# Performance work log

Hardware: AMD Instinct MI355X
Metric: run time of the kernel (lower is better)

## Reference

```python
import jax, jax.numpy as jnp
import numpy as np

SR = 10  # self.sr in the torch module

def _linear_params(key, fan_in, fan_out):
    kw, kb = jax.random.split(key)
    bound = 1.0 / np.sqrt(fan_in)
    W = jax.random.uniform(kw, (fan_out, fan_in), jnp.float32, -bound, bound)
    b = jax.random.uniform(kb, (fan_out,), jnp.float32, -bound, bound)
    return W, b

def setup_inputs() -> dict:
    key = jax.random.key(0)
    ks = jax.random.split(key, 6)
    P, H = 2048, 1024
    R = C = P * SR
    X = jax.random.normal(ks[0], (R, C), jnp.float32)
    p = jax.random.randint(ks[1], (P,), 0, 64, jnp.int32)
    W1, b1 = _linear_params(ks[2], 1, H)
    W2, b2 = _linear_params(ks[3], H, H)
    W3, b3 = _linear_params(ks[4], H, H)
    W4, b4 = _linear_params(ks[5], H, 1)
    return {"X": X, "p": p, "W1": W1, "b1": b1, "W2": W2, "b2": b2,
            "W3": W3, "b3": b3, "W4": W4, "b4": b4}

def _forward(X, p, W1, b1, W2, b2, W3, b3, W4, b4):
    P = p.shape[0]
    C = X.shape[1]
    # shift_rows: only rows i*SR for i in [0, P-2] are populated; all other
    # rows of the shifted matrix are NaN and contribute 0 sum / 0 count below.
    rows = X[jnp.arange(P - 1) * SR]                      # (P-1, C)
    shifts = p[: P - 1]
    # torch.roll(x, s): out[j] = x[(j - s) mod C]
    cols = (jnp.arange(C)[None, :] - shifts[:, None]) % C  # (P-1, C)
    shifted = jnp.take_along_axis(rows, cols, axis=1)      # (P-1, C)
    # nan_mean over rows (NaN rows of the full matrix drop out identically)
    mask = jnp.isnan(shifted)
    col_sum = jnp.where(mask, 0.0, shifted).sum(axis=0)
    col_cnt = (~mask).sum(axis=0).astype(jnp.float32)
    m = jnp.where(col_cnt > 0, col_sum / col_cnt, jnp.float32(jnp.nan))  # (C,)
    # fill_nan_with_last_value: serial forward-fill (index 0 kept as-is)
    def step(last, xi):
        v = jnp.where(jnp.isnan(xi), last, xi)
        return v, v
    _, rest = jax.lax.scan(step, m[0], m[1:])
    filled = jnp.concatenate([m[:1], rest])                # (C,)
    x = filled[::SR][:P][:, None]                          # (P, 1)
    h = jax.nn.relu(x @ W1.T + b1)
    h = jax.nn.relu(h @ W2.T + b2)
    h = jax.nn.relu(h @ W3.T + b3)
    y = h @ W4.T + b4                                      # (P, 1)
    return y[:, 0]

def reference(X, p, W1, b1, W2, b2, W3, b3, W4, b4):
    return _forward(X, p, W1, b1, W2, b2, W3, b3, W4, b4)
```

## Files before the change

kernel.cpp:

```cpp
#include <hip/hip_runtime.h>
#include <hip/hip_bf16.h>

#define CC 20480
#define PP 2048
#define NROWS 2047
#define SRR 10
#define HH 1024
#define NCH 64

typedef __attribute__((ext_vector_type(8))) short short8;
typedef __attribute__((ext_vector_type(4))) float f32x4;

__device__ __forceinline__ void split_bf16(float v, unsigned short& hi, unsigned short& lo) {
    __hip_bfloat16 h = __float2bfloat16(v);
    float r = v - __bfloat162float(h);
    __hip_bfloat16 l2 = __float2bfloat16(r);
    hi = *(unsigned short*)&h;
    lo = *(unsigned short*)&l2;
}

__global__ __launch_bounds__(256) void pre_k(const float* __restrict__ X,
                                             const int* __restrict__ p,
                                             float* __restrict__ psum,
                                             const float* __restrict__ W2,
                                             unsigned short* __restrict__ w2h,
                                             unsigned short* __restrict__ w2l,
                                             const float* __restrict__ W3,
                                             unsigned short* __restrict__ w3h,
                                             unsigned short* __restrict__ w3l) {
    int b = blockIdx.x, t = threadIdx.x;
    if (b < 512) {
        int k = (b & 7) * 256 + t;
        int chunk = b >> 3;
        int r0 = chunk * 32;
        int r1 = r0 + 32; if (r1 > NROWS) r1 = NROWS;
        float s = 0.f;
        int base = SRR * k;
        for (int i = r0; i < r1; ++i) {
            int col = base - p[i]; if (col < 0) col += CC;
            s += X[(size_t)i * (size_t)(SRR * CC) + col];
        }
        psum[chunk * PP + k] = s;
        return;
    }
    int bb = b - 512;
    const float* src; unsigned short *dh, *dl;
    if (bb < 256) { src = W2; dh = w2h; dl = w2l; }
    else { src = W3; dh = w3h; dl = w3l; bb -= 256; }
    int idx = bb * 4096 + t * 16;
    #pragma unroll
    for (int q = 0; q < 4; ++q) {
        float4 v = *(const float4*)&src[idx + q * 4];
        float vv[4] = {v.x, v.y, v.z, v.w};
        ushort hi4[4], lo4[4];
        #pragma unroll
        for (int i = 0; i < 4; ++i) split_bf16(vv[i], hi4[i], lo4[i]);
        *(ushort4*)&dh[idx + q * 4] = *(ushort4*)hi4;
        *(ushort4*)&dl[idx + q * 4] = *(ushort4*)lo4;
    }
}

__device__ __forceinline__ void gload16(const unsigned short* g, unsigned short* lds) {
    __builtin_amdgcn_global_load_lds(
        (const __attribute__((address_space(1))) void*)g,
        (__attribute__((address_space(3))) void*)lds,
        16, 0, 0);
}

#define BM 128
#define BN 64
#define BK 64

__global__ __launch_bounds__(512, 2) void gemm1_k(
    const float* __restrict__ psum,
    const float* __restrict__ W1, const float* __restrict__ b1,
    const unsigned short* __restrict__ Bh, const unsigned short* __restrict__ Bl,
    const float* __restrict__ b2,
    unsigned short* __restrict__ Ch, unsigned short* __restrict__ Cl)
{
    __shared__ unsigned short Bb[3][8192];
    __shared__ float w1f[1024], b1f[1024], xv[128];

    int lin = blockIdx.x;
    int v = (lin & 7) * 32 + (lin >> 3);
    int bx = v >> 4, by = v & 15;
    int bm = bx * BM, bn = by * BN;
    int t = threadIdx.x, w = t >> 6, l = t & 63;
    int lr = l & 15, lk = l >> 4;
    int wr = w >> 1, wc = w & 1;

    size_t offB = (size_t)(bn + (w >> 1) * 16 + lr) * HH + (w & 1) * 32 + lk * 8;
#define BSTAGE(buf, k0)                                         \
    do {                                                        \
        gload16(Bh + offB + (k0), Bb[buf] + w * 512);           \
        gload16(Bl + offB + (k0), Bb[buf] + 4096 + w * 512);    \
    } while (0)

    BSTAGE(0, 0);
    {
        int row = t >> 2, q = t & 3;
        float s = 0.f;
        #pragma unroll
        for (int j = 0; j < 16; ++j) s += psum[(q * 16 + j) * PP + bm + row];
        s += __shfl_xor(s, 1, 64);
        s += __shfl_xor(s, 2, 64);
        if (q == 0) xv[row] = s * (1.0f / (float)NROWS);
        if (t < 256) *(float4*)&w1f[t * 4] = *(const float4*)&W1[t * 4];
        else *(float4*)&b1f[(t - 256) * 4] = *(const float4*)&b1[(t - 256) * 4];
    }
    __syncthreads();

    float x0 = xv[wr * 32 + lr], x1 = xv[wr * 32 + 16 + lr];

    f32x4 acc[2][2];
    #pragma unroll
    for (int i = 0; i < 2; ++i)
        #pragma unroll
        for (int j = 0; j < 2; ++j) acc[i][j] = (f32x4)(0.f);

    int nt = HH / BK;
    for (int tt = 0; tt < nt; ++tt) {
        int cur = tt % 3;
        if (tt + 1 < nt) {
            BSTAGE((tt + 1) % 3, (tt + 1) * BK);
            asm volatile("s_waitcnt vmcnt(2)" ::: "memory");
        } else {
            asm volatile("s_waitcnt vmcnt(0)" ::: "memory");
        }
        __builtin_amdgcn_s_barrier();
        __builtin_amdgcn_sched_barrier(0);
        __builtin_amdgcn_s_setprio(1);
        #pragma unroll
        for (int s2 = 0; s2 < 2; ++s2) {
            int k0 = tt * BK + s2 * 32;
            float4 wva = *(const float4*)&w1f[k0 + lk * 8];
            float4 wvb = *(const float4*)&w1f[k0 + lk * 8 + 4];
            float4 bva = *(const float4*)&b1f[k0 + lk * 8];
            float4 bvb = *(const float4*)&b1f[k0 + lk * 8 + 4];
            float wv[8] = {wva.x, wva.y, wva.z, wva.w, wvb.x, wvb.y, wvb.z, wvb.w};
            float bv2[8] = {bva.x, bva.y, bva.z, bva.w, bvb.x, bvb.y, bvb.z, bvb.w};
            ushort ahh[2][8], all2[2][8];
            #pragma unroll
            for (int mi = 0; mi < 2; ++mi) {
                float xm = mi ? x1 : x0;
                #pragma unroll
                for (int j = 0; j < 8; ++j) {
                    float h = fmaf(xm, wv[j], bv2[j]);
                    h = h > 0.f ? h : 0.f;
                    split_bf16(h, ahh[mi][j], all2[mi][j]);
                }
            }
            short8 bh2[2], bl2[2];
            #pragma unroll
            for (int ni = 0; ni < 2; ++ni) {
                bh2[ni] = *(const short8*)&Bb[cur][((wc * 2 + ni) * 2 + s2) * 512 + l * 8];
                bl2[ni] = *(const short8*)&Bb[cur][4096 + ((wc * 2 + ni) * 2 + s2) * 512 + l * 8];
            }
            #pragma unroll
            for (int mi = 0; mi < 2; ++mi) {
                short8 ah2 = *(short8*)ahh[mi];
                short8 al2 = *(short8*)all2[mi];
                #pragma unroll
                for (int ni = 0; ni < 2; ++ni) {
                    acc[mi][ni] = __builtin_amdgcn_mfma_f32_16x16x32_bf16(ah2, bh2[ni], acc[mi][ni], 0, 0, 0);
                    acc[mi][ni] = __builtin_amdgcn_mfma_f32_16x16x32_bf16(ah2, bl2[ni], acc[mi][ni], 0, 0, 0);
                    acc[mi][ni] = __builtin_amdgcn_mfma_f32_16x16x32_bf16(al2, bh2[ni], acc[mi][ni], 0, 0, 0);
                }
            }
        }
        __builtin_amdgcn_s_setprio(0);
        __builtin_amdgcn_sched_barrier(0);
    }
#undef BSTAGE

    float bv[2];
    #pragma unroll
    for (int ni = 0; ni < 2; ++ni) bv[ni] = b2[bn + wc * 32 + ni * 16 + lr];
    #pragma unroll
    for (int mi = 0; mi < 2; ++mi)
        #pragma unroll
        for (int ni = 0; ni < 2; ++ni)
            #pragma unroll
            for (int r = 0; r < 4; ++r) {
                int row = bm + wr * 32 + mi * 16 + lk * 4 + r;
                int col = bn + wc * 32 + ni * 16 + lr;
                float vv = acc[mi][ni][r] + bv[ni];
                vv = vv > 0.f ? vv : 0.f;
                unsigned short hi, lo;
                split_bf16(vv, hi, lo);
                Ch[(size_t)row * HH + col] = hi;
                Cl[(size_t)row * HH + col] = lo;
            }
}

__global__ __launch_bounds__(512, 2) void gemm2_k(
    const unsigned short* __restrict__ Ah, const unsigned short* __restrict__ Al,
    const unsigned short* __restrict__ Bh, const unsigned short* __restrict__ Bl,
    const float* __restrict__ b3,
    const float* __restrict__ W4, float* __restrict__ partial)
{
    __shared__ unsigned short lds[3][24576];
    int lin = blockIdx.x;
    int v = (lin & 7) * 32 + (lin >> 3);
    int bx = v >> 4, by = v & 15;
    int bm = bx * BM, bn = by * BN;
    int t = threadIdx.x, w = t >> 6, l = t & 63;
    int lr = l & 15, lk = l >> 4;
    int wr = w >> 1, wc = w & 1;

    size_t offA = (size_t)(bm + w * 16 + lr) * HH + lk * 8;
    size_t offB = (size_t)(bn + (w & 3) * 16 + lr) * HH + lk * 8;

#define STAGE(buf, k0)                                                          \
    do {                                                                        \
        unsigned short* L = lds[buf];                                           \
        gload16(Ah + offA + (k0),      L + (w * 2 + 0) * 512);                  \
        gload16(Ah + offA + (k0) + 32, L + (w * 2 + 1) * 512);                  \
        gload16(Al + offA + (k0),      L + 8192 + (w * 2 + 0) * 512);           \
        gload16(Al + offA + (k0) + 32, L + 8192 + (w * 2 + 1) * 512);           \
        if (w < 4) {                                                            \
            gload16(Bh + offB + (k0),      L + 16384 + ((w & 3) * 2 + 0) * 512);\
            gload16(Bh + offB + (k0) + 32, L + 16384 + ((w & 3) * 2 + 1) * 512);\
        } else {                                                                \
            gload16(Bl + offB + (k0),      L + 20480 + ((w & 3) * 2 + 0) * 512);\
            gload16(Bl + offB + (k0) + 32, L + 20480 + ((w & 3) * 2 + 1) * 512);\
        }                                                                       \
    } while (0)

    f32x4 acc[2][2];
    #pragma unroll
    for (int i = 0; i < 2; ++i)
        #pragma unroll
        for (int j = 0; j < 2; ++j) acc[i][j] = (f32x4)(0.f);

    STAGE(0, 0);

    int nt = HH / BK;
    for (int tt = 0; tt < nt; ++tt) {
        int cur = tt % 3;
        if (tt + 1 < nt) {
            STAGE((tt + 1) % 3, (tt + 1) * BK);
            asm volatile("s_waitcnt vmcnt(6)" ::: "memory");
        } else {
            asm volatile("s_waitcnt vmcnt(0)" ::: "memory");
        }
        __builtin_amdgcn_s_barrier();
        __builtin_amdgcn_sched_barrier(0);
        __builtin_amdgcn_s_setprio(1);
        unsigned short* L = lds[cur];
        #pragma unroll
        for (int s2 = 0; s2 < 2; ++s2) {
            short8 ah2[2], al2[2], bh2[2], bl2[2];
            #pragma unroll
            for (int mi = 0; mi < 2; ++mi) {
                ah2[mi] = *(const short8*)&L[((wr * 2 + mi) * 2 + s2) * 512 + l * 8];
                al2[mi] = *(const short8*)&L[8192 + ((wr * 2 + mi) * 2 + s2) * 512 + l * 8];
            }
            #pragma unroll
            for (int ni = 0; ni < 2; ++ni) {
                bh2[ni] = *(const short8*)&L[16384 + ((wc * 2 + ni) * 2 + s2) * 512 + l * 8];
                bl2[ni] = *(const short8*)&L[20480 + ((wc * 2 + ni) * 2 + s2) * 512 + l * 8];
            }
            #pragma unroll
            for (int mi = 0; mi < 2; ++mi)
                #pragma unroll
                for (int ni = 0; ni < 2; ++ni) {
                    acc[mi][ni] = __builtin_amdgcn_mfma_f32_16x16x32_bf16(ah2[mi], bh2[ni], acc[mi][ni], 0, 0, 0);
                    acc[mi][ni] = __builtin_amdgcn_mfma_f32_16x16x32_bf16(ah2[mi], bl2[ni], acc[mi][ni], 0, 0, 0);
                    acc[mi][ni] = __builtin_amdgcn_mfma_f32_16x16x32_bf16(al2[mi], bh2[ni], acc[mi][ni], 0, 0, 0);
                }
        }
        __builtin_amdgcn_s_setprio(0);
        __builtin_amdgcn_sched_barrier(0);
    }
#undef STAGE

    float bv[2], w4v[2];
    #pragma unroll
    for (int ni = 0; ni < 2; ++ni) {
        bv[ni]  = b3[bn + wc * 32 + ni * 16 + lr];
        w4v[ni] = W4[bn + wc * 32 + ni * 16 + lr];
    }
    #pragma unroll
    for (int mi = 0; mi < 2; ++mi) {
        float ps[4];
        #pragma unroll
        for (int r = 0; r < 4; ++r) {
            float acc_d = 0.f;
            #pragma unroll
            for (int ni = 0; ni < 2; ++ni) {
                float vv = acc[mi][ni][r] + bv[ni];
                vv = vv > 0.f ? vv : 0.f;
                acc_d += vv * w4v[ni];
            }
            ps[r] = acc_d;
        }
        #pragma unroll
        for (int r = 0; r < 4; ++r) {
            #pragma unroll
            for (int m2 = 1; m2 < 16; m2 <<= 1) ps[r] += __shfl_xor(ps[r], m2, 64);
        }
        if (lr == 0) {
            #pragma unroll
            for (int r = 0; r < 4; ++r) {
                int row = bm + wr * 32 + mi * 16 + lk * 4 + r;
                partial[(size_t)row * 32 + by * 2 + wc] = ps[r];
            }
        }
    }
}

__global__ __launch_bounds__(256) void ysum_k(const float* __restrict__ partial,
                                              const float* __restrict__ b4,
                                              float* __restrict__ y) {
    int r = blockIdx.x * 256 + threadIdx.x;
    float s = 0.f;
    #pragma unroll
    for (int q = 0; q < 8; ++q) {
        float4 v = *(const float4*)&partial[(size_t)r * 32 + q * 4];
        s += v.x + v.y + v.z + v.w;
    }
    y[r] = s + b4[0];
}

extern "C" void kernel_launch(void* const* d_in, const int* in_sizes, int n_in,
                              void* d_out, int out_size, void* d_ws, size_t ws_size,
                              hipStream_t stream) {
    const float* X  = (const float*)d_in[0];
    const int*   p  = (const int*)d_in[1];
    const float* W1 = (const float*)d_in[2];
    const float* b1 = (const float*)d_in[3];
    const float* W2 = (const float*)d_in[4];
    const float* b2 = (const float*)d_in[5];
    const float* W3 = (const float*)d_in[6];
    const float* b3 = (const float*)d_in[7];
    const float* W4 = (const float*)d_in[8];
    const float* b4 = (const float*)d_in[9];
    float* out = (float*)d_out;

    char* ws = (char*)d_ws;
    size_t off = 0;
    float* psum = (float*)(ws + off); off += (size_t)NCH * PP * 4;
    unsigned short* h2h = (unsigned short*)(ws + off); off += (size_t)PP * HH * 2;
    unsigned short* h2l = (unsigned short*)(ws + off); off += (size_t)PP * HH * 2;
    unsigned short* w2h = (unsigned short*)(ws + off); off += (size_t)HH * HH * 2;
    unsigned short* w2l = (unsigned short*)(ws + off); off += (size_t)HH * HH * 2;
    unsigned short* w3h = (unsigned short*)(ws + off); off += (size_t)HH * HH * 2;
    unsigned short* w3l = (unsigned short*)(ws + off); off += (size_t)HH * HH * 2;
    float* partial = (float*)(ws + off); off += (size_t)PP * 32 * 4;

    pre_k<<<1024, 256, 0, stream>>>(X, p, psum, W2, w2h, w2l, W3, w3h, w3l);
    gemm1_k<<<256, 512, 0, stream>>>(psum, W1, b1, w2h, w2l, b2, h2h, h2l);
    gemm2_k<<<256, 512, 0, stream>>>(h2h, h2l, w3h, w3l, b3, W4, partial);
    ysum_k<<<PP / 256, 256, 0, stream>>>(partial, b4, out);
}
```

Measured before the change: 80.19 us.

## Move W3 bf16 split into gemm1 launch and deepen GEMM prefetch to two stages

After: 83.76 us. 4.5% more time.

```diff
diff --git a/kernel.cpp b/kernel.cpp
--- a/kernel.cpp
+++ b/kernel.cpp
@@ -24,10 +24,7 @@
                                              float* __restrict__ psum,
                                              const float* __restrict__ W2,
                                              unsigned short* __restrict__ w2h,
-                                             unsigned short* __restrict__ w2l,
-                                             const float* __restrict__ W3,
-                                             unsigned short* __restrict__ w3h,
-                                             unsigned short* __restrict__ w3l) {
+                                             unsigned short* __restrict__ w2l) {
     int b = blockIdx.x, t = threadIdx.x;
     if (b < 512) {
         int k = (b & 7) * 256 + t;
@@ -44,19 +41,16 @@
         return;
     }
     int bb = b - 512;
-    const float* src; unsigned short *dh, *dl;
-    if (bb < 256) { src = W2; dh = w2h; dl = w2l; }
-    else { src = W3; dh = w3h; dl = w3l; bb -= 256; }
     int idx = bb * 4096 + t * 16;
     #pragma unroll
     for (int q = 0; q < 4; ++q) {
-        float4 v = *(const float4*)&src[idx + q * 4];
+        float4 v = *(const float4*)&W2[idx + q * 4];
         float vv[4] = {v.x, v.y, v.z, v.w};
         ushort hi4[4], lo4[4];
         #pragma unroll
         for (int i = 0; i < 4; ++i) split_bf16(vv[i], hi4[i], lo4[i]);
-        *(ushort4*)&dh[idx + q * 4] = *(ushort4*)hi4;
-        *(ushort4*)&dl[idx + q * 4] = *(ushort4*)lo4;
+        *(ushort4*)&w2h[idx + q * 4] = *(ushort4*)hi4;
+        *(ushort4*)&w2l[idx + q * 4] = *(ushort4*)lo4;
     }
 }
 
@@ -76,16 +70,33 @@
     const float* __restrict__ W1, const float* __restrict__ b1,
     const unsigned short* __restrict__ Bh, const unsigned short* __restrict__ Bl,
     const float* __restrict__ b2,
-    unsigned short* __restrict__ Ch, unsigned short* __restrict__ Cl)
+    unsigned short* __restrict__ Ch, unsigned short* __restrict__ Cl,
+    const float* __restrict__ W3,
+    unsigned short* __restrict__ w3h, unsigned short* __restrict__ w3l)
 {
     __shared__ unsigned short Bb[3][8192];
     __shared__ float w1f[1024], b1f[1024], xv[128];
 
-    int lin = blockIdx.x;
+    int lin = blockIdx.x, t = threadIdx.x;
+    if (lin >= 256) {
+        int bb = lin - 256;
+        int idx = bb * 4096 + t * 8;
+        #pragma unroll
+        for (int q = 0; q < 2; ++q) {
+            float4 v = *(const float4*)&W3[idx + q * 4];
+            float vv[4] = {v.x, v.y, v.z, v.w};
+            ushort hi4[4], lo4[4];
+            #pragma unroll
+            for (int i = 0; i < 4; ++i) split_bf16(vv[i], hi4[i], lo4[i]);
+            *(ushort4*)&w3h[idx + q * 4] = *(ushort4*)hi4;
+            *(ushort4*)&w3l[idx + q * 4] = *(ushort4*)lo4;
+        }
+        return;
+    }
     int v = (lin & 7) * 32 + (lin >> 3);
     int bx = v >> 4, by = v & 15;
     int bm = bx * BM, bn = by * BN;
-    int t = threadIdx.x, w = t >> 6, l = t & 63;
+    int w = t >> 6, l = t & 63;
     int lr = l & 15, lk = l >> 4;
     int wr = w >> 1, wc = w & 1;
 
@@ -97,6 +108,7 @@
     } while (0)
 
     BSTAGE(0, 0);
+    BSTAGE(1, BK);
     {
         int row = t >> 2, q = t & 3;
         float s = 0.f;
@@ -121,14 +133,11 @@
     int nt = HH / BK;
     for (int tt = 0; tt < nt; ++tt) {
         int cur = tt % 3;
-        if (tt + 1 < nt) {
-            BSTAGE((tt + 1) % 3, (tt + 1) * BK);
-            asm volatile("s_waitcnt vmcnt(2)" ::: "memory");
-        } else {
-            asm volatile("s_waitcnt vmcnt(0)" ::: "memory");
-        }
+        if (tt + 1 < nt) asm volatile("s_waitcnt vmcnt(2)" ::: "memory");
+        else             asm volatile("s_waitcnt vmcnt(0)" ::: "memory");
         __builtin_amdgcn_s_barrier();
         __builtin_amdgcn_sched_barrier(0);
+        if (tt + 2 < nt) BSTAGE((tt + 2) % 3, (tt + 2) * BK);
         __builtin_amdgcn_s_setprio(1);
         #pragma unroll
         for (int s2 = 0; s2 < 2; ++s2) {
@@ -234,18 +243,16 @@
         for (int j = 0; j < 2; ++j) acc[i][j] = (f32x4)(0.f);
 
     STAGE(0, 0);
+    STAGE(1, BK);
 
     int nt = HH / BK;
     for (int tt = 0; tt < nt; ++tt) {
         int cur = tt % 3;
-        if (tt + 1 < nt) {
-            STAGE((tt + 1) % 3, (tt + 1) * BK);
-            asm volatile("s_waitcnt vmcnt(6)" ::: "memory");
-        } else {
-            asm volatile("s_waitcnt vmcnt(0)" ::: "memory");
-        }
+        if (tt + 1 < nt) asm volatile("s_waitcnt vmcnt(6)" ::: "memory");
+        else             asm volatile("s_waitcnt vmcnt(0)" ::: "memory");
         __builtin_amdgcn_s_barrier();
         __builtin_amdgcn_sched_barrier(0);
+        if (tt + 2 < nt) STAGE((tt + 2) % 3, (tt + 2) * BK);
         __builtin_amdgcn_s_setprio(1);
         unsigned short* L = lds[cur];
         #pragma unroll
@@ -349,8 +356,8 @@
     unsigned short* w3l = (unsigned short*)(ws + off); off += (size_t)HH * HH * 2;
     float* partial = (float*)(ws + off); off += (size_t)PP * 32 * 4;
 
-    pre_k<<<1024, 256, 0, stream>>>(X, p, psum, W2, w2h, w2l, W3, w3h, w3l);
-    gemm1_k<<<256, 512, 0, stream>>>(psum, W1, b1, w2h, w2l, b2, h2h, h2l);
+    pre_k<<<768, 256, 0, stream>>>(X, p, psum, W2, w2h, w2l);
+    gemm1_k<<<512, 512, 0, stream>>>(psum, W1, b1, w2h, w2l, b2, h2h, h2l, W3, w3h, w3l);
     gemm2_k<<<256, 512, 0, stream>>>(h2h, h2l, w3h, w3l, b3, W4, partial);
     ysum_k<<<PP / 256, 256, 0, stream>>>(partial, b4, out);
 }
```

## Fuse all four stages into one cooperative kernel with grid-wide syncs

Applied to the files above, without the earlier changes.

Result: slower. 185.1 us (+130.9%).

```diff
diff --git a/kernel.cpp b/kernel.cpp
--- a/kernel.cpp
+++ b/kernel.cpp
@@ -1,5 +1,8 @@
 #include <hip/hip_runtime.h>
+#include <hip/hip_cooperative_groups.h>
 #include <hip/hip_bf16.h>
+
+namespace cg = cooperative_groups;
 
 #define CC 20480
 #define PP 2048
@@ -19,19 +22,37 @@
     lo = *(unsigned short*)&l2;
 }
 
-__global__ __launch_bounds__(256) void pre_k(const float* __restrict__ X,
-                                             const int* __restrict__ p,
-                                             float* __restrict__ psum,
-                                             const float* __restrict__ W2,
-                                             unsigned short* __restrict__ w2h,
-                                             unsigned short* __restrict__ w2l,
-                                             const float* __restrict__ W3,
-                                             unsigned short* __restrict__ w3h,
-                                             unsigned short* __restrict__ w3l) {
+__device__ __forceinline__ void gload16(const unsigned short* g, unsigned short* lds) {
+    __builtin_amdgcn_global_load_lds(
+        (const __attribute__((address_space(1))) void*)g,
+        (__attribute__((address_space(3))) void*)lds,
+        16, 0, 0);
+}
+
+#define BM 128
+#define BN 64
+#define BK 64
+
+__global__ __launch_bounds__(512, 1) void fused_k(
+    const float* __restrict__ X, const int* __restrict__ p,
+    float* __restrict__ psum,
+    const float* __restrict__ W1, const float* __restrict__ b1,
+    const float* __restrict__ W2, const float* __restrict__ b2,
+    const float* __restrict__ W3, const float* __restrict__ b3,
+    const float* __restrict__ W4, const float* __restrict__ b4,
+    unsigned short* __restrict__ w2h, unsigned short* __restrict__ w2l,
+    unsigned short* __restrict__ w3h, unsigned short* __restrict__ w3l,
+    unsigned short* __restrict__ h2h, unsigned short* __restrict__ h2l,
+    float* __restrict__ partial, float* __restrict__ out)
+{
+    __shared__ unsigned short LDSU[3][24576];
+    cg::grid_group grid = cg::this_grid();
     int b = blockIdx.x, t = threadIdx.x;
-    if (b < 512) {
-        int k = (b & 7) * 256 + t;
-        int chunk = b >> 3;
+    int tid = b * 512 + t;
+
+    {
+        int k = tid & 2047;
+        int chunk = tid >> 11;
         int r0 = chunk * 32;
         int r1 = r0 + 32; if (r1 > NROWS) r1 = NROWS;
         float s = 0.f;
@@ -41,286 +62,265 @@
             s += X[(size_t)i * (size_t)(SRR * CC) + col];
         }
         psum[chunk * PP + k] = s;
-        return;
+        int idx = tid * 8;
+        #pragma unroll
+        for (int q = 0; q < 2; ++q) {
+            float4 v2 = *(const float4*)&W2[idx + q * 4];
+            float4 v3 = *(const float4*)&W3[idx + q * 4];
+            float a2[4] = {v2.x, v2.y, v2.z, v2.w};
+            float a3[4] = {v3.x, v3.y, v3.z, v3.w};
+            ushort h24[4], l24[4], h34[4], l34[4];
+            #pragma unroll
+            for (int i = 0; i < 4; ++i) {
+                split_bf16(a2[i], h24[i], l24[i]);
+                split_bf16(a3[i], h34[i], l34[i]);
+            }
+            *(ushort4*)&w2h[idx + q * 4] = *(ushort4*)h24;
+            *(ushort4*)&w2l[idx + q * 4] = *(ushort4*)l24;
+            *(ushort4*)&w3h[idx + q * 4] = *(ushort4*)h34;
+            *(ushort4*)&w3l[idx + q * 4] = *(ushort4*)l34;
+        }
     }
-    int bb = b - 512;
-    const float* src; unsigned short *dh, *dl;
-    if (bb < 256) { src = W2; dh = w2h; dl = w2l; }
-    else { src = W3; dh = w3h; dl = w3l; bb -= 256; }
-    int idx = bb * 4096 + t * 16;
-    #pragma unroll
-    for (int q = 0; q < 4; ++q) {
-        float4 v = *(const float4*)&src[idx + q * 4];
-        float vv[4] = {v.x, v.y, v.z, v.w};
-        ushort hi4[4], lo4[4];
-        #pragma unroll
-        for (int i = 0; i < 4; ++i) split_bf16(vv[i], hi4[i], lo4[i]);
-        *(ushort4*)&dh[idx + q * 4] = *(ushort4*)hi4;
-        *(ushort4*)&dl[idx + q * 4] = *(ushort4*)lo4;
+    grid.sync();
+
+    {
+        unsigned short* BbF = &LDSU[0][0];
+        float* w1f = (float*)(BbF + 3 * 8192);
+        float* b1f = w1f + 1024;
+        float* xv  = b1f + 1024;
+
+        int v = (b & 7) * 32 + (b >> 3);
+        int bx = v >> 4, by = v & 15;
+        int bm = bx * BM, bn = by * BN;
+        int w = t >> 6, l = t & 63;
+        int lr = l & 15, lk = l >> 4;
+        int wr = w >> 1, wc = w & 1;
+
+        size_t offB = (size_t)(bn + (w >> 1) * 16 + lr) * HH + (w & 1) * 32 + lk * 8;
+#define BSTAGE(buf, k0)                                                \
+        do {                                                           \
+            gload16(w2h + offB + (k0), BbF + (buf) * 8192 + w * 512);  \
+            gload16(w2l + offB + (k0), BbF + (buf) * 8192 + 4096 + w * 512); \
+        } while (0)
+
+        BSTAGE(0, 0);
+        {
+            int row = t >> 2, q = t & 3;
+            float s = 0.f;
+            #pragma unroll
+            for (int j = 0; j < 16; ++j) s += psum[(q * 16 + j) * PP + bm + row];
+            s += __shfl_xor(s, 1, 64);
+            s += __shfl_xor(s, 2, 64);
+            if (q == 0) xv[row] = s * (1.0f / (float)NROWS);
+            if (t < 256) *(float4*)&w1f[t * 4] = *(const float4*)&W1[t * 4];
+            else *(float4*)&b1f[(t - 256) * 4] = *(const float4*)&b1[(t - 256) * 4];
+        }
+        __syncthreads();
+
+        float x0 = xv[wr * 32 + lr], x1 = xv[wr * 32 + 16 + lr];
+
+        f32x4 acc[2][2];
+        #pragma unroll
+        for (int i = 0; i < 2; ++i)
+            #pragma unroll
+            for (int j = 0; j < 2; ++j) acc[i][j] = (f32x4)(0.f);
+
+        int nt = HH / BK;
+        for (int tt = 0; tt < nt; ++tt) {
+            int cur = tt % 3;
+            if (tt + 1 < nt) {
+                BSTAGE((tt + 1) % 3, (tt + 1) * BK);
+                asm volatile("s_waitcnt vmcnt(2)" ::: "memory");
+            } else {
+                asm volatile("s_waitcnt vmcnt(0)" ::: "memory");
+            }
+            __builtin_amdgcn_s_barrier();
+            __builtin_amdgcn_sched_barrier(0);
+            __builtin_amdgcn_s_setprio(1);
+            #pragma unroll
+            for (int s2 = 0; s2 < 2; ++s2) {
+                int k0 = tt * BK + s2 * 32;
+                float4 wva = *(const float4*)&w1f[k0 + lk * 8];
+                float4 wvb = *(const float4*)&w1f[k0 + lk * 8 + 4];
+                float4 bva = *(const float4*)&b1f[k0 + lk * 8];
+                float4 bvb = *(const float4*)&b1f[k0 + lk * 8 + 4];
+                float wv[8] = {wva.x, wva.y, wva.z, wva.w, wvb.x, wvb.y, wvb.z, wvb.w};
+                float bv2[8] = {bva.x, bva.y, bva.z, bva.w, bvb.x, bvb.y, bvb.z, bvb.w};
+                ushort ahh[2][8], all2[2][8];
+                #pragma unroll
+                for (int mi = 0; mi < 2; ++mi) {
+                    float xm = mi ? x1 : x0;
+                    #pragma unroll
+                    for (int j = 0; j < 8; ++j) {
+                        float h = fmaf(xm, wv[j], bv2[j]);
+                        h = h > 0.f ? h : 0.f;
+                        split_bf16(h, ahh[mi][j], all2[mi][j]);
+                    }
+                }
+                short8 bh2[2], bl2[2];
+                #pragma unroll
+                for (int ni = 0; ni < 2; ++ni) {
+                    bh2[ni] = *(const short8*)&BbF[cur * 8192 + ((wc * 2 + ni) * 2 + s2) * 512 + l * 8];
+                    bl2[ni] = *(const short8*)&BbF[cur * 8192 + 4096 + ((wc * 2 + ni) * 2 + s2) * 512 + l * 8];
+                }
+                #pragma unroll
+                for (int mi = 0; mi < 2; ++mi) {
+                    short8 ah2 = *(short8*)ahh[mi];
+                    short8 al2 = *(short8*)all2[mi];
+                    #pragma unroll
+                    for (int ni = 0; ni < 2; ++ni) {
+                        acc[mi][ni] = __builtin_amdgcn_mfma_f32_16x16x32_bf16(ah2, bh2[ni], acc[mi][ni], 0, 0, 0);
+                        acc[mi][ni] = __builtin_amdgcn_mfma_f32_16x16x32_bf16(ah2, bl2[ni], acc[mi][ni], 0, 0, 0);
+                        acc[mi][ni] = __builtin_amdgcn_mfma_f32_16x16x32_bf16(al2, bh2[ni], acc[mi][ni], 0, 0, 0);
+                    }
+                }
+            }
+            __builtin_amdgcn_s_setprio(0);
+            __builtin_amdgcn_sched_barrier(0);
+        }
+#undef BSTAGE
+
+        float bv[2];
+        #pragma unroll
+        for (int ni = 0; ni < 2; ++ni) bv[ni] = b2[bn + wc * 32 + ni * 16 + lr];
+        #pragma unroll
+        for (int mi = 0; mi < 2; ++mi)
+            #pragma unroll
+            for (int ni = 0; ni < 2; ++ni)
+                #pragma unroll
+                for (int r = 0; r < 4; ++r) {
+                    int row = bm + wr * 32 + mi * 16 + lk * 4 + r;
+                    int col = bn + wc * 32 + ni * 16 + lr;
+                    float vv = acc[mi][ni][r] + bv[ni];
+                    vv = vv > 0.f ? vv : 0.f;
+                    unsigned short hi, lo;
+                    split_bf16(vv, hi, lo);
+                    h2h[(size_t)row * HH + col] = hi;
+                    h2l[(size_t)row * HH + col] = lo;
+                }
     }
-}
-
-__device__ __forceinline__ void gload16(const unsigned short* g, unsigned short* lds) {
-    __builtin_amdgcn_global_load_lds(
-        (const __attribute__((address_space(1))) void*)g,
-        (__attribute__((address_space(3))) void*)lds,
-        16, 0, 0);
-}
-
-#define BM 128
-#define BN 64
-#define BK 64
-
-__global__ __launch_bounds__(512, 2) void gemm1_k(
-    const float* __restrict__ psum,
-    const float* __restrict__ W1, const float* __restrict__ b1,
-    const unsigned short* __restrict__ Bh, const unsigned short* __restrict__ Bl,
-    const float* __restrict__ b2,
-    unsigned short* __restrict__ Ch, unsigned short* __restrict__ Cl)
-{
-    __shared__ unsigned short Bb[3][8192];
-    __shared__ float w1f[1024], b1f[1024], xv[128];
-
-    int lin = blockIdx.x;
-    int v = (lin & 7) * 32 + (lin >> 3);
-    int bx = v >> 4, by = v & 15;
-    int bm = bx * BM, bn = by * BN;
-    int t = threadIdx.x, w = t >> 6, l = t & 63;
-    int lr = l & 15, lk = l >> 4;
-    int wr = w >> 1, wc = w & 1;
-
-    size_t offB = (size_t)(bn + (w >> 1) * 16 + lr) * HH + (w & 1) * 32 + lk * 8;
-#define BSTAGE(buf, k0)                                         \
-    do {                                                        \
-        gload16(Bh + offB + (k0), Bb[buf] + w * 512);           \
-        gload16(Bl + offB + (k0), Bb[buf] + 4096 + w * 512);    \
-    } while (0)
-
-    BSTAGE(0, 0);
+    grid.sync();
+
     {
-        int row = t >> 2, q = t & 3;
+        int v = (b & 7) * 32 + (b >> 3);
+        int bx = v >> 4, by = v & 15;
+        int bm = bx * BM, bn = by * BN;
+        int w = t >> 6, l = t & 63;
+        int lr = l & 15, lk = l >> 4;
+        int wr = w >> 1, wc = w & 1;
+
+        size_t offA = (size_t)(bm + w * 16 + lr) * HH + lk * 8;
+        size_t offB = (size_t)(bn + (w & 3) * 16 + lr) * HH + lk * 8;
+
+#define STAGE(buf, k0)                                                              \
+        do {                                                                        \
+            unsigned short* L = LDSU[buf];                                          \
+            gload16(h2h + offA + (k0),      L + (w * 2 + 0) * 512);                 \
+            gload16(h2h + offA + (k0) + 32, L + (w * 2 + 1) * 512);                 \
+            gload16(h2l + offA + (k0),      L + 8192 + (w * 2 + 0) * 512);          \
+            gload16(h2l + offA + (k0) + 32, L + 8192 + (w * 2 + 1) * 512);          \
+            if (w < 4) {                                                            \
+                gload16(w3h + offB + (k0),      L + 16384 + ((w & 3) * 2 + 0) * 512);\
+                gload16(w3h + offB + (k0) + 32, L + 16384 + ((w & 3) * 2 + 1) * 512);\
+            } else {                                                                \
+                gload16(w3l + offB + (k0),      L + 20480 + ((w & 3) * 2 + 0) * 512);\
+                gload16(w3l + offB + (k0) + 32, L + 20480 + ((w & 3) * 2 + 1) * 512);\
+            }                                                                       \
+        } while (0)
+
+        f32x4 acc[2][2];
+        #pragma unroll
+        for (int i = 0; i < 2; ++i)
+            #pragma unroll
+            for (int j = 0; j < 2; ++j) acc[i][j] = (f32x4)(0.f);
+
+        STAGE(0, 0);
+
+        int nt = HH / BK;
+        for (int tt = 0; tt < nt; ++tt) {
+            int cur = tt % 3;
+            if (tt + 1 < nt) {
+                STAGE((tt + 1) % 3, (tt + 1) * BK);
+                asm volatile("s_waitcnt vmcnt(6)" ::: "memory");
+            } else {
+                asm volatile("s_waitcnt vmcnt(0)" ::: "memory");
+            }
+            __builtin_amdgcn_s_barrier();
+            __builtin_amdgcn_sched_barrier(0);
+            __builtin_amdgcn_s_setprio(1);
+            unsigned short* L = LDSU[cur];
+            #pragma unroll
+            for (int s2 = 0; s2 < 2; ++s2) {
+                short8 ah2[2], al2[2], bh2[2], bl2[2];
+                #pragma unroll
+                for (int mi = 0; mi < 2; ++mi) {
+                    ah2[mi] = *(const short8*)&L[((wr * 2 + mi) * 2 + s2) * 512 + l * 8];
+                    al2[mi] = *(const short8*)&L[8192 + ((wr * 2 + mi) * 2 + s2) * 512 + l * 8];
+                }
+                #pragma unroll
+                for (int ni = 0; ni < 2; ++ni) {
+                    bh2[ni] = *(const short8*)&L[16384 + ((wc * 2 + ni) * 2 + s2) * 512 + l * 8];
+                    bl2[ni] = *(const short8*)&L[20480 + ((wc * 2 + ni) * 2 + s2) * 512 + l * 8];
+                }
+                #pragma unroll
+                for (int mi = 0; mi < 2; ++mi)
+                    #pragma unroll
+                    for (int ni = 0; ni < 2; ++ni) {
+                        acc[mi][ni] = __builtin_amdgcn_mfma_f32_16x16x32_bf16(ah2[mi], bh2[ni], acc[mi][ni], 0, 0, 0);
+                        acc[mi][ni] = __builtin_amdgcn_mfma_f32_16x16x32_bf16(ah2[mi], bl2[ni], acc[mi][ni], 0, 0, 0);
+                        acc[mi][ni] = __builtin_amdgcn_mfma_f32_16x16x32_bf16(al2[mi], bh2[ni], acc[mi][ni], 0, 0, 0);
+                    }
+            }
+            __builtin_amdgcn_s_setprio(0);
+            __builtin_amdgcn_sched_barrier(0);
+        }
+#undef STAGE
+
+        float bv[2], w4v[2];
+        #pragma unroll
+        for (int ni = 0; ni < 2; ++ni) {
+            bv[ni]  = b3[bn + wc * 32 + ni * 16 + lr];
+            w4v[ni] = W4[bn + wc * 32 + ni * 16 + lr];
+        }
+        #pragma unroll
+        for (int mi = 0; mi < 2; ++mi) {
+            float ps[4];
+            #pragma unroll
+            for (int r = 0; r < 4; ++r) {
+                float acc_d = 0.f;
+                #pragma unroll
+                for (int ni = 0; ni < 2; ++ni) {
+                    float vv = acc[mi][ni][r] + bv[ni];
+                    vv = vv > 0.f ? vv : 0.f;
+                    acc_d += vv * w4v[ni];
+                }
+                ps[r] = acc_d;
+            }
+            #pragma unroll
+            for (int r = 0; r < 4; ++r) {
+                #pragma unroll
+                for (int m2 = 1; m2 < 16; m2 <<= 1) ps[r] += __shfl_xor(ps[r], m2, 64);
+            }
+            if (lr == 0) {
+                #pragma unroll
+                for (int r = 0; r < 4; ++r) {
+                    int row = bm + wr * 32 + mi * 16 + lk * 4 + r;
+                    partial[(size_t)row * 32 + by * 2 + wc] = ps[r];
+                }
+            }
+        }
+    }
+    grid.sync();
+
+    if (tid < PP) {
         float s = 0.f;
         #pragma unroll
-        for (int j = 0; j < 16; ++j) s += psum[(q * 16 + j) * PP + bm + row];
-        s += __shfl_xor(s, 1, 64);
-        s += __shfl_xor(s, 2, 64);
-        if (q == 0) xv[row] = s * (1.0f / (float)NROWS);
-        if (t < 256) *(float4*)&w1f[t * 4] = *(const float4*)&W1[t * 4];
-        else *(float4*)&b1f[(t - 256) * 4] = *(const float4*)&b1[(t - 256) * 4];
+        for (int q = 0; q < 8; ++q) {
+            float4 v = *(const float4*)&partial[(size_t)tid * 32 + q * 4];
+            s += v.x + v.y + v.z + v.w;
+        }
+        out[tid] = s + b4[0];
     }
-    __syncthreads();
-
-    float x0 = xv[wr * 32 + lr], x1 = xv[wr * 32 + 16 + lr];
-
-    f32x4 acc[2][2];
-    #pragma unroll
-    for (int i = 0; i < 2; ++i)
-        #pragma unroll
-        for (int j = 0; j < 2; ++j) acc[i][j] = (f32x4)(0.f);
-
-    int nt = HH / BK;
-    for (int tt = 0; tt < nt; ++tt) {
-        int cur = tt % 3;
-        if (tt + 1 < nt) {
-            BSTAGE((tt + 1) % 3, (tt + 1) * BK);
-            asm volatile("s_waitcnt vmcnt(2)" ::: "memory");
-        } else {
-            asm volatile("s_waitcnt vmcnt(0)" ::: "memory");
-        }
-        __builtin_amdgcn_s_barrier();
-        __builtin_amdgcn_sched_barrier(0);
-        __builtin_amdgcn_s_setprio(1);
-        #pragma unroll
-        for (int s2 = 0; s2 < 2; ++s2) {
-            int k0 = tt * BK + s2 * 32;
-            float4 wva = *(const float4*)&w1f[k0 + lk * 8];
-            float4 wvb = *(const float4*)&w1f[k0 + lk * 8 + 4];
-            float4 bva = *(const float4*)&b1f[k0 + lk * 8];
-            float4 bvb = *(const float4*)&b1f[k0 + lk * 8 + 4];
-            float wv[8] = {wva.x, wva.y, wva.z, wva.w, wvb.x, wvb.y, wvb.z, wvb.w};
-            float bv2[8] = {bva.x, bva.y, bva.z, bva.w, bvb.x, bvb.y, bvb.z, bvb.w};
-            ushort ahh[2][8], all2[2][8];
-            #pragma unroll
-            for (int mi = 0; mi < 2; ++mi) {
-                float xm = mi ? x1 : x0;
-                #pragma unroll
-                for (int j = 0; j < 8; ++j) {
-                    float h = fmaf(xm, wv[j], bv2[j]);
-                    h = h > 0.f ? h : 0.f;
-                    split_bf16(h, ahh[mi][j], all2[mi][j]);
-                }
-            }
-            short8 bh2[2], bl2[2];
-            #pragma unroll
-            for (int ni = 0; ni < 2; ++ni) {
-                bh2[ni] = *(const short8*)&Bb[cur][((wc * 2 + ni) * 2 + s2) * 512 + l * 8];
-                bl2[ni] = *(const short8*)&Bb[cur][4096 + ((wc * 2 + ni) * 2 + s2) * 512 + l * 8];
-            }
-            #pragma unroll
-            for (int mi = 0; mi < 2; ++mi) {
-                short8 ah2 = *(short8*)ahh[mi];
-                short8 al2 = *(short8*)all2[mi];
-                #pragma unroll
-                for (int ni = 0; ni < 2; ++ni) {
-                    acc[mi][ni] = __builtin_amdgcn_mfma_f32_16x16x32_bf16(ah2, bh2[ni], acc[mi][ni], 0, 0, 0);
-                    acc[mi][ni] = __builtin_amdgcn_mfma_f32_16x16x32_bf16(ah2, bl2[ni], acc[mi][ni], 0, 0, 0);
-                    acc[mi][ni] = __builtin_amdgcn_mfma_f32_16x16x32_bf16(al2, bh2[ni], acc[mi][ni], 0, 0, 0);
-                }
-            }
-        }
-        __builtin_amdgcn_s_setprio(0);
-        __builtin_amdgcn_sched_barrier(0);
-    }
-#undef BSTAGE
-
-    float bv[2];
-    #pragma unroll
-    for (int ni = 0; ni < 2; ++ni) bv[ni] = b2[bn + wc * 32 + ni * 16 + lr];
-    #pragma unroll
-    for (int mi = 0; mi < 2; ++mi)
-        #pragma unroll
-        for (int ni = 0; ni < 2; ++ni)
-            #pragma unroll
-            for (int r = 0; r < 4; ++r) {
-                int row = bm + wr * 32 + mi * 16 + lk * 4 + r;
-                int col = bn + wc * 32 + ni * 16 + lr;
-                float vv = acc[mi][ni][r] + bv[ni];
-                vv = vv > 0.f ? vv : 0.f;
-                unsigned short hi, lo;
-                split_bf16(vv, hi, lo);
-                Ch[(size_t)row * HH + col] = hi;
-                Cl[(size_t)row * HH + col] = lo;
-            }
-}
-
-__global__ __launch_bounds__(512, 2) void gemm2_k(
-    const unsigned short* __restrict__ Ah, const unsigned short* __restrict__ Al,
-    const unsigned short* __restrict__ Bh, const unsigned short* __restrict__ Bl,
-    const float* __restrict__ b3,
-    const float* __restrict__ W4, float* __restrict__ partial)
-{
-    __shared__ unsigned short lds[3][24576];
-    int lin = blockIdx.x;
-    int v = (lin & 7) * 32 + (lin >> 3);
-    int bx = v >> 4, by = v & 15;
-    int bm = bx * BM, bn = by * BN;
-    int t = threadIdx.x, w = t >> 6, l = t & 63;
-    int lr = l & 15, lk = l >> 4;
-    int wr = w >> 1, wc = w & 1;
-
-    size_t offA = (size_t)(bm + w * 16 + lr) * HH + lk * 8;
-    size_t offB = (size_t)(bn + (w & 3) * 16 + lr) * HH + lk * 8;
-
-#define STAGE(buf, k0)                                                          \
-    do {                                                                        \
-        unsigned short* L = lds[buf];                                           \
-        gload16(Ah + offA + (k0),      L + (w * 2 + 0) * 512);                  \
-        gload16(Ah + offA + (k0) + 32, L + (w * 2 + 1) * 512);                  \
-        gload16(Al + offA + (k0),      L + 8192 + (w * 2 + 0) * 512);           \
-        gload16(Al + offA + (k0) + 32, L + 8192 + (w * 2 + 1) * 512);           \
-        if (w < 4) {                                                            \
-            gload16(Bh + offB + (k0),      L + 16384 + ((w & 3) * 2 + 0) * 512);\
-            gload16(Bh + offB + (k0) + 32, L + 16384 + ((w & 3) * 2 + 1) * 512);\
-        } else {                                                                \
-            gload16(Bl + offB + (k0),      L + 20480 + ((w & 3) * 2 + 0) * 512);\
-            gload16(Bl + offB + (k0) + 32, L + 20480 + ((w & 3) * 2 + 1) * 512);\
-        }                                                                       \
-    } while (0)
-
-    f32x4 acc[2][2];
-    #pragma unroll
-    for (int i = 0; i < 2; ++i)
-        #pragma unroll
-        for (int j = 0; j < 2; ++j) acc[i][j] = (f32x4)(0.f);
-
-    STAGE(0, 0);
-
-    int nt = HH / BK;
-    for (int tt = 0; tt < nt; ++tt) {
-        int cur = tt % 3;
-        if (tt + 1 < nt) {
-            STAGE((tt + 1) % 3, (tt + 1) * BK);
-            asm volatile("s_waitcnt vmcnt(6)" ::: "memory");
-        } else {
-            asm volatile("s_waitcnt vmcnt(0)" ::: "memory");
-        }
-        __builtin_amdgcn_s_barrier();
-        __builtin_amdgcn_sched_barrier(0);
-        __builtin_amdgcn_s_setprio(1);
-        unsigned short* L = lds[cur];
-        #pragma unroll
-        for (int s2 = 0; s2 < 2; ++s2) {
-            short8 ah2[2], al2[2], bh2[2], bl2[2];
-            #pragma unroll
-            for (int mi = 0; mi < 2; ++mi) {
-                ah2[mi] = *(const short8*)&L[((wr * 2 + mi) * 2 + s2) * 512 + l * 8];
-                al2[mi] = *(const short8*)&L[8192 + ((wr * 2 + mi) * 2 + s2) * 512 + l * 8];
-            }
-            #pragma unroll
-            for (int ni = 0; ni < 2; ++ni) {
-                bh2[ni] = *(const short8*)&L[16384 + ((wc * 2 + ni) * 2 + s2) * 512 + l * 8];
-                bl2[ni] = *(const short8*)&L[20480 + ((wc * 2 + ni) * 2 + s2) * 512 + l * 8];
-            }
-            #pragma unroll
-            for (int mi = 0; mi < 2; ++mi)
-                #pragma unroll
-                for (int ni = 0; ni < 2; ++ni) {
-                    acc[mi][ni] = __builtin_amdgcn_mfma_f32_16x16x32_bf16(ah2[mi], bh2[ni], acc[mi][ni], 0, 0, 0);
-                    acc[mi][ni] = __builtin_amdgcn_mfma_f32_16x16x32_bf16(ah2[mi], bl2[ni], acc[mi][ni], 0, 0, 0);
-                    acc[mi][ni] = __builtin_amdgcn_mfma_f32_16x16x32_bf16(al2[mi], bh2[ni], acc[mi][ni], 0, 0, 0);
-                }
-        }
-        __builtin_amdgcn_s_setprio(0);
-        __builtin_amdgcn_sched_barrier(0);
-    }
-#undef STAGE
-
-    float bv[2], w4v[2];
-    #pragma unroll
-    for (int ni = 0; ni < 2; ++ni) {
-        bv[ni]  = b3[bn + wc * 32 + ni * 16 + lr];
-        w4v[ni] = W4[bn + wc * 32 + ni * 16 + lr];
-    }
-    #pragma unroll
-    for (int mi = 0; mi < 2; ++mi) {
-        float ps[4];
-        #pragma unroll
-        for (int r = 0; r < 4; ++r) {
-            float acc_d = 0.f;
-            #pragma unroll
-            for (int ni = 0; ni < 2; ++ni) {
-                float vv = acc[mi][ni][r] + bv[ni];
-                vv = vv > 0.f ? vv : 0.f;
-                acc_d += vv * w4v[ni];
-            }
-            ps[r] = acc_d;
-        }
-        #pragma unroll
-        for (int r = 0; r < 4; ++r) {
-            #pragma unroll
-            for (int m2 = 1; m2 < 16; m2 <<= 1) ps[r] += __shfl_xor(ps[r], m2, 64);
-        }
-        if (lr == 0) {
-            #pragma unroll
-            for (int r = 0; r < 4; ++r) {
-                int row = bm + wr * 32 + mi * 16 + lk * 4 + r;
-                partial[(size_t)row * 32 + by * 2 + wc] = ps[r];
-            }
-        }
-    }
-}
-
-__global__ __launch_bounds__(256) void ysum_k(const float* __restrict__ partial,
-                                              const float* __restrict__ b4,
-                                              float* __restrict__ y) {
-    int r = blockIdx.x * 256 + threadIdx.x;
-    float s = 0.f;
-    #pragma unroll
-    for (int q = 0; q < 8; ++q) {
-        float4 v = *(const float4*)&partial[(size_t)r * 32 + q * 4];
-        s += v.x + v.y + v.z + v.w;
-    }
-    y[r] = s + b4[0];
 }
 
 extern "C" void kernel_launch(void* const* d_in, const int* in_sizes, int n_in,
@@ -349,8 +349,12 @@
     unsigned short* w3l = (unsigned short*)(ws + off); off += (size_t)HH * HH * 2;
     float* partial = (float*)(ws + off); off += (size_t)PP * 32 * 4;
 
-    pre_k<<<1024, 256, 0, stream>>>(X, p, psum, W2, w2h, w2l, W3, w3h, w3l);
-    gemm1_k<<<256, 512, 0, stream>>>(psum, W1, b1, w2h, w2l, b2, h2h, h2l);
-    gemm2_k<<<256, 512, 0, stream>>>(h2h, h2l, w3h, w3l, b3, W4, partial);
-    ysum_k<<<PP / 256, 256, 0, stream>>>(partial, b4, out);
+    void* args[] = {
+        (void*)&X, (void*)&p, (void*)&psum,
+        (void*)&W1, (void*)&b1, (void*)&W2, (void*)&b2,
+        (void*)&W3, (void*)&b3, (void*)&W4, (void*)&b4,
+        (void*)&w2h, (void*)&w2l, (void*)&w3h, (void*)&w3l,
+        (void*)&h2h, (void*)&h2l, (void*)&partial, (void*)&out
+    };
+    hipLaunchCooperativeKernel((void*)fused_k, dim3(256), dim3(512), args, 0, stream);
 }
```
